# Performance work log

Measured on AMD Instinct MI355X. Metric: run time of the kernel, lower is better.

Reference implementation:

```python
import jax, jax.numpy as jnp
import numpy as np

EPS = 1e-5

def knn_idx(x, k):
    # x: (B,C,N). Returns (B,N,k) indices of k nearest neighbors (by L2).
    inner = -2.0 * jnp.einsum('bcn,bcm->bnm', x, x)          # (B,N,N)
    xx = jnp.sum(x * x, axis=1)                               # (B,N)
    neg_dist = -xx[:, :, None] - inner - xx[:, None, :]       # (B,N,N)
    _, idx = jax.lax.top_k(neg_dist, k)                       # (B,N,k)
    return idx

def get_graph_features(x, k):
    # x: (B,C,N) -> (B,2C,N,k) with channels = concat(neighbor-center, center)
    B, C, N = x.shape
    idx = knn_idx(x, k)                                       # (B,N,k)
    pts = jnp.transpose(x, (0, 2, 1))                         # (B,N,C)
    nbr = jax.vmap(lambda p, i: p[i])(pts, idx)               # (B,N,k,C)
    ctr = jnp.broadcast_to(pts[:, :, None, :], nbr.shape)     # (B,N,k,C)
    feat = jnp.concatenate([nbr - ctr, ctr], axis=-1)         # (B,N,k,2C)
    return jnp.transpose(feat, (0, 3, 1, 2))                  # (B,2C,N,k)

def conv_bn_relu(y, W, gamma, beta):
    # 1x1 conv (pointwise matmul) + train-mode BatchNorm2d + ReLU
    y = jnp.einsum('oc,bcnk->bonk', W, y)
    mean = jnp.mean(y, axis=(0, 2, 3), keepdims=True)
    var = jnp.var(y, axis=(0, 2, 3), keepdims=True)
    yhat = (y - mean) * jax.lax.rsqrt(var + EPS)
    return jax.nn.relu(yhat * gamma[None, :, None, None] + beta[None, :, None, None])

def setup_inputs() -> dict:
    key = jax.random.key(0)
    ks = jax.random.split(key, 16)
    B, N, k, emb = 8, 2048, 20, 512
    x = jax.random.normal(ks[0], (B, 3, N), dtype=jnp.float32)
    def w(kk, o, c):
        return jax.random.normal(kk, (o, c), dtype=jnp.float32) * (1.0 / np.sqrt(c))
    inp = {
        'x': x, 'k': k,
        'W1': w(ks[1], 64, 6),   'W2': w(ks[2], 64, 64),
        'W3': w(ks[3], 128, 64), 'W4': w(ks[4], 256, 128),
        'W5': w(ks[5], emb, 512),
    }
    for i, c in zip(range(1, 6), [64, 64, 128, 256, emb]):
        inp[f'g{i}'] = 1.0 + 0.1 * jax.random.normal(ks[5 + i], (c,), dtype=jnp.float32)
        inp[f'b{i}'] = 0.1 * jax.random.normal(ks[10 + i], (c,), dtype=jnp.float32)
    return inp

def reference(x, W1, W2, W3, W4, W5, g1, b1, g2, b2, g3, b3, g4, b4, g5, b5, k):
    B, C, N = x.shape
    h = get_graph_features(x, k)                  # (B,6,N,k)
    h = conv_bn_relu(h, W1, g1, b1)               # (B,64,N,k)
    x1 = jnp.max(h, axis=-1, keepdims=True)
    h = conv_bn_relu(h, W2, g2, b2)               # (B,64,N,k)
    x2 = jnp.max(h, axis=-1, keepdims=True)
    h = conv_bn_relu(h, W3, g3, b3)               # (B,128,N,k)
    x3 = jnp.max(h, axis=-1, keepdims=True)
    h = conv_bn_relu(h, W4, g4, b4)               # (B,256,N,k)
    x4 = jnp.max(h, axis=-1, keepdims=True)
    cat = jnp.concatenate([x1, x2, x3, x4], axis=1)  # (B,512,N,1)
    out = conv_bn_relu(cat, W5, g5, b5)              # (B,emb,N,1)
    return out.reshape(B, -1, N)
```

## Files before the change

kernel.cpp:

```cpp
#include <hip/hip_runtime.h>
#include <hip/hip_bf16.h>

typedef __hip_bfloat16 bf16;
typedef __attribute__((ext_vector_type(8))) short short8v;
typedef __attribute__((ext_vector_type(4))) float f32x4;
typedef unsigned int uint;
typedef unsigned long long u64;

#define BATCH 8
#define NPTS 2048
#define KNN 20
#define NK (NPTS*KNN)
#define P4 (BATCH*NK)
#define BN_TOT (BATCH*NPTS)

union BU { bf16 h; unsigned short u; };
__device__ __forceinline__ unsigned short f2bf(float f){
    BU bu; bu.h = __float2bfloat16(f); return bu.u;
}
__device__ __forceinline__ float bfu2f(unsigned short u){
    return __uint_as_float(((uint)u) << 16);
}
__device__ __forceinline__ uint fenc(float f){
    uint b = __float_as_uint(f);
    return (b & 0x80000000u) ? ~b : (b | 0x80000000u);
}

__global__ void initK(float* __restrict__ shadow)
{
    int t = blockIdx.x*256 + threadIdx.x;
    if (t < 5*16*1024) shadow[t] = 0.f;
}

__global__ void cvtWS(const float* __restrict__ src, short* __restrict__ dst, int Cin)
{
    int t = blockIdx.x*256 + threadIdx.x;
    int co = t / Cin, ci = t - co*Cin;
    dst[(size_t)co*Cin + (ci ^ ((co & 7) << 3))] = (short)f2bf(src[t]);
}

__global__ __launch_bounds__(512)
void knn_kernel(const float* __restrict__ x, int* __restrict__ idx)
{
    #pragma clang fp contract(off)
    __shared__ float4 sp[NPTS];
    const int b  = blockIdx.x / (NPTS/8);
    const int nb = blockIdx.x % (NPTS/8);
    const float* xb = x + (size_t)b*3*NPTS;
    for (int i = threadIdx.x; i < NPTS; i += 512) {
        float y0 = xb[i], y1 = xb[NPTS+i], y2 = xb[2*NPTS+i];
        float4 p; p.x = y0; p.y = y1; p.z = y2;
        p.w = y0*y0 + y1*y1 + y2*y2;
        sp[i] = p;
    }
    __syncthreads();

    const int wave = threadIdx.x >> 6;
    const int lane = threadIdx.x & 63;
    const int n = nb*8 + wave;

    const float4 pn = sp[n];
    const float x0 = pn.x, x1 = pn.y, x2 = pn.z;
    const float xxn = pn.w;

    constexpr int L = 4;
    float bA[L], bB[L]; int iA[L], iB[L];
    #pragma unroll
    for (int i = 0; i < L; ++i) {
        bA[i] = -3e38f; bB[i] = -3e38f; iA[i] = 0x7fffffff; iB[i] = 0x7fffffff;
    }

    float4 c0 = sp[lane], c1 = sp[lane + 64];
    #pragma unroll
    for (int t = 0; t < NPTS/128; ++t) {
        float4 n0, n1;
        if (t + 1 < NPTS/128) {
            n0 = sp[lane + (2*t+2)*64];
            n1 = sp[lane + (2*t+3)*64];
        }
        int m0 = lane + (2*t)*64, m1 = m0 + 64;
        float dot0 = x0*c0.x + x1*c0.y + x2*c0.z;
        float v0 = -xxn - (-2.f*dot0) - c0.w;
        float dot1 = x0*c1.x + x1*c1.y + x2*c1.z;
        float v1 = -xxn - (-2.f*dot1) - c1.w;
        int mi0 = m0, mi1 = m1;
        #pragma unroll
        for (int i = 0; i < L; ++i) {
            { bool sw = v0 > bA[i];
              float tv = sw ? bA[i] : v0; int ti = sw ? iA[i] : mi0;
              bA[i] = sw ? v0 : bA[i]; iA[i] = sw ? mi0 : iA[i]; v0 = tv; mi0 = ti; }
            { bool sw = v1 > bB[i];
              float tv = sw ? bB[i] : v1; int ti = sw ? iB[i] : mi1;
              bB[i] = sw ? v1 : bB[i]; iB[i] = sw ? mi1 : iB[i]; v1 = tv; mi1 = ti; }
        }
        c0 = n0; c1 = n1;
    }

    u64 kA[L], kB[L];
    #pragma unroll
    for (int i = 0; i < L; ++i) {
        kA[i] = ((u64)fenc(bA[i]) << 32) | (uint)(~iA[i]);
        kB[i] = ((u64)fenc(bB[i]) << 32) | (uint)(~iB[i]);
    }

    size_t obase = ((size_t)b*NPTS + n)*KNN;
    int popA = 0, popB = 0;
    #pragma unroll 1
    for (int s = 0; s < KNN; ++s) {
        bool useA = kA[0] >= kB[0];
        u64 my = useA ? kA[0] : kB[0];
        u64 g = my;
        #pragma unroll
        for (int off = 1; off < 64; off <<= 1) {
            u64 o = __shfl_xor(g, off);
            g = (o > g) ? o : g;
        }
        if (lane == 0) idx[obase + s] = (int)(~(uint)g);
        bool win = (my == g);
        bool pA = win && useA, pB = win && !useA;
        #pragma unroll
        for (int i = 0; i < L-1; ++i) {
            kA[i] = pA ? kA[i+1] : kA[i];
            kB[i] = pB ? kB[i+1] : kB[i];
        }
        kA[L-1] = pA ? 0ULL : kA[L-1];
        kB[L-1] = pB ? 0ULL : kB[L-1];
        popA += pA; popB += pB;
    }

    if (__any((popA >= L) || (popB >= L))) {
        float B[KNN]; int BI[KNN];
        #pragma unroll
        for (int i = 0; i < KNN; ++i) { B[i] = -3e38f; BI[i] = 0x7fffffff; }
        #pragma unroll 1
        for (int j = 0; j < NPTS/64; ++j) {
            int m = lane + j*64;
            float4 p = sp[m];
            float dot = x0*p.x + x1*p.y + x2*p.z;
            float v = -xxn - (-2.f*dot) - p.w;
            int mi = m;
            #pragma unroll
            for (int i = 0; i < KNN; ++i) {
                bool sw = v > B[i];
                float tv = sw ? B[i]  : v;
                int   ti = sw ? BI[i] : mi;
                B[i]  = sw ? v  : B[i];
                BI[i] = sw ? mi : BI[i];
                v = tv; mi = ti;
            }
        }
        #pragma unroll 1
        for (int s = 0; s < KNN; ++s) {
            float mv = B[0]; int mi = BI[0];
            #pragma unroll
            for (int off = 1; off < 64; off <<= 1) {
                float ov = __shfl_xor(mv, off);
                int   oi = __shfl_xor(mi, off);
                if (ov > mv || (ov == mv && oi < mi)) { mv = ov; mi = oi; }
            }
            bool win = (B[0] == mv) && (BI[0] == mi);
            #pragma unroll
            for (int i = 0; i < KNN-1; ++i) {
                B[i]  = win ? B[i+1]  : B[i];
                BI[i] = win ? BI[i+1] : BI[i];
            }
            B[KNN-1]  = win ? -3e38f     : B[KNN-1];
            BI[KNN-1] = win ? 0x7fffffff : BI[KNN-1];
            if (lane == 0) idx[obase + s] = mi;
        }
    }
}

__global__ __launch_bounds__(256)
void conv1T(const float* __restrict__ x, const int* __restrict__ idx,
            const float* __restrict__ W1, bf16* __restrict__ h1,
            float* __restrict__ shadow)
{
    __shared__ unsigned short lv[256][64];
    __shared__ float ps[4][64], pq[4][64];
    const int tid = threadIdx.x;
    int p = blockIdx.x*256 + tid;
    int b = p / NK;
    int r = p - b*NK;
    int n = r / KNN;
    int j = idx[p];
    const float* xb = x + (size_t)b*3*NPTS;
    float c0 = xb[n], c1 = xb[NPTS+n], c2 = xb[2*NPTS+n];
    float d0 = xb[j]-c0, d1 = xb[NPTS+j]-c1, d2 = xb[2*NPTS+j]-c2;
    uint4* outp = reinterpret_cast<uint4*>(reinterpret_cast<unsigned short*>(h1) + (size_t)p*64);
    uint4* lrow = reinterpret_cast<uint4*>(lv[tid]);
    #pragma unroll
    for (int ch = 0; ch < 8; ++ch) {
        uint u[4];
        #pragma unroll
        for (int q = 0; q < 4; ++q) {
            const float* wa = W1 + (ch*8 + q*2)*6;
            float a0 = wa[0]*d0 + wa[1]*d1 + wa[2]*d2 + wa[3]*c0 + wa[4]*c1 + wa[5]*c2;
            const float* wb = wa + 6;
            float a1 = wb[0]*d0 + wb[1]*d1 + wb[2]*d2 + wb[3]*c0 + wb[4]*c1 + wb[5]*c2;
            u[q] = (uint)f2bf(a0) | ((uint)f2bf(a1) << 16);
        }
        uint4 val = make_uint4(u[0], u[1], u[2], u[3]);
        outp[ch] = val;
        lrow[ch] = val;
    }
    __syncthreads();
    int c = tid & 63, grp = tid >> 6;
    float s = 0.f, q = 0.f;
    #pragma unroll 8
    for (int i = 0; i < 64; ++i) {
        float v = bfu2f(lv[grp*64 + i][c]);
        s += v; q += v*v;
    }
    ps[grp][c] = s; pq[grp][c] = q;
    __syncthreads();
    if (tid < 64) {
        float S = ps[0][tid]+ps[1][tid]+ps[2][tid]+ps[3][tid];
        float Q = pq[0][tid]+pq[1][tid]+pq[2][tid]+pq[3][tid];
        float* sh = shadow + (size_t)(blockIdx.x & 15)*1024;
        atomicAdd(&sh[tid], S);
        atomicAdd(&sh[512 + tid], Q);
    }
}

__global__ void fin_kernel(const float* __restrict__ shadow,
                           const float* __restrict__ gamma, const float* __restrict__ beta,
                           float* __restrict__ scbiF, int C, float invCnt)
{
    for (int c = threadIdx.x; c < C; c += 256) {
        float s = 0.f, q = 0.f;
        #pragma unroll
        for (int i = 0; i < 16; ++i) { s += shadow[i*1024 + c]; q += shadow[i*1024 + 512 + c]; }
        float m = s*invCnt;
        float var = q*invCnt - m*m;
        float rs = rsqrtf(var + 1e-5f);
        float sc = rs * gamma[c];
        float bi = fmaf(-m, sc, beta[c]);
        scbiF[2*c] = sc; scbiF[2*c+1] = bi;
    }
}

template<int Cout, int Cin, int M, int POOL, int NSPLIT, int KTILE, int BT, int PF>
__global__ __launch_bounds__(BT)
void gemmT(const short* __restrict__ Wb, const bf16* __restrict__ in,
           bf16* __restrict__ outT, float* __restrict__ shadow,
           float* __restrict__ pmax, float* __restrict__ pmin)
{
    constexpr int CSPL = Cout/NSPLIT;
    constexpr int NT   = CSPL/16;
    constexpr int ROWS = (BT/64)*16*M;
    constexpr int KSTOT = Cin/32;
    constexpr int KPT   = KTILE/32;
    constexpr int NTILE = Cin/KTILE;
    constexpr int NG    = POOL ? ROWS/KNN : 1;
    constexpr size_t WB = (size_t)CSPL*KTILE*2;
    constexpr size_t PB = POOL ? (size_t)2*ROWS*17*4 : 0;
    constexpr size_t SB = WB > PB ? WB : PB;

    __shared__ __align__(16) char smem[SB];
    short* WsmS = reinterpret_cast<short*>(smem);
    float* poolF = reinterpret_cast<float*>(smem);

    const int tid  = threadIdx.x;
    const int lane = tid & 63;
    const int g = lane >> 4, mr = lane & 15;
    const int wid = tid >> 6;
    const int rowBlk = blockIdx.x*ROWS;
    const int rowW   = rowBlk + wid*(16*M);
    const int ntBase = blockIdx.y*CSPL;
    const short* inS = reinterpret_cast<const short*>(in);

    f32x4 acc[M][NT];
    #pragma unroll
    for (int m = 0; m < M; ++m)
    #pragma unroll
    for (int i = 0; i < NT; ++i) acc[m][i] = (f32x4){0.f,0.f,0.f,0.f};

    short8v a[M], anext[M];
    if (PF) {
        #pragma unroll
        for (int m = 0; m < M; ++m)
            a[m] = *reinterpret_cast<const short8v*>(inS + (size_t)(rowW + m*16 + mr)*Cin + 8*g);
    }

    #pragma unroll 1
    for (int kt = 0; kt < NTILE; ++kt) {
        if (kt) __syncthreads();
        {
            const int ktBase = kt*KTILE;
            for (int f8 = tid; f8 < CSPL*KTILE/8; f8 += BT) {
                int f = f8*8;
                int row = f / KTILE, col = f - row*KTILE;
                short8v v = *reinterpret_cast<const short8v*>(
                    Wb + (size_t)(ntBase + row)*Cin + ktBase + col);
                *reinterpret_cast<short8v*>(WsmS + f) = v;
            }
        }
        __syncthreads();

        #pragma unroll
        for (int ksl = 0; ksl < KPT; ++ksl) {
            const int ksg = kt*KPT + ksl;
            const int k0 = ksg*32 + 8*g;
            if (!PF) {
                #pragma unroll
                for (int m = 0; m < M; ++m)
                    a[m] = *reinterpret_cast<const short8v*>(inS + (size_t)(rowW + m*16 + mr)*Cin + k0);
            } else if (ksg + 1 < KSTOT) {
                #pragma unroll
                for (int m = 0; m < M; ++m)
                    anext[m] = *reinterpret_cast<const short8v*>(inS + (size_t)(rowW + m*16 + mr)*Cin + k0 + 32);
            }
            const int kx = ksl*32 + 8*g;
            #pragma unroll
            for (int nt = 0; nt < NT; ++nt) {
                const int brow = nt*16 + mr;
                short8v bfr = *reinterpret_cast<const short8v*>(
                    WsmS + brow*KTILE + (kx ^ ((mr & 7) << 3)));
                #pragma unroll
                for (int m = 0; m < M; ++m)
                    acc[m][nt] = __builtin_amdgcn_mfma_f32_16x16x32_bf16(a[m], bfr, acc[m][nt], 0, 0, 0);
            }
            if (PF) {
                #pragma unroll
                for (int m = 0; m < M; ++m) a[m] = anext[m];
            }
        }
    }

    float* sh = shadow + (size_t)((blockIdx.x ^ blockIdx.y) & 15)*1024;
    #pragma unroll
    for (int nt = 0; nt < NT; ++nt) {
        float s = 0.f, q = 0.f;
        #pragma unroll
        for (int m = 0; m < M; ++m)
        #pragma unroll
        for (int j = 0; j < 4; ++j) { float v = acc[m][nt][j]; s += v; q += v*v; }
        s += __shfl_xor(s, 16); s += __shfl_xor(s, 32);
        q += __shfl_xor(q, 16); q += __shfl_xor(q, 32);
        if (g == 0) {
            atomicAdd(&sh[ntBase + nt*16 + mr], s);
            atomicAdd(&sh[512 + ntBase + nt*16 + mr], q);
        }
    }

    if (!POOL) {
        #pragma unroll
        for (int m = 0; m < M; ++m)
        #pragma unroll
        for (int nt = 0; nt < NT; ++nt)
        #pragma unroll
        for (int j = 0; j < 4; ++j) {
            size_t row = (size_t)rowW + m*16 + g*4 + j;
            outT[row*Cout + ntBase + nt*16 + mr] = __float2bfloat16(acc[m][nt][j]);
        }
    } else {
        __syncthreads();
        #pragma unroll
        for (int np = 0; np < NT/2; ++np) {
            #pragma unroll
            for (int hh = 0; hh < 2; ++hh) {
                #pragma unroll
                for (int m = 0; m < M; ++m)
                #pragma unroll
                for (int j = 0; j < 4; ++j) {
                    int row = wid*(16*M) + m*16 + g*4 + j;
                    poolF[hh*(ROWS*17) + row*17 + mr] = acc[m][np*2+hh][j];
                }
            }
            __syncthreads();
            if (tid < 2*NG*16) {
                int hh = tid / (NG*16);
                int gg = (tid >> 4) % NG;
                int cc = tid & 15;
                float mx = -3e38f, mn = 3e38f;
                #pragma unroll
                for (int kk = 0; kk < KNN; ++kk) {
                    float v = poolF[hh*(ROWS*17) + (gg*KNN + kk)*17 + cc];
                    mx = fmaxf(mx, v); mn = fminf(mn, v);
                }
                int grp = rowBlk/KNN + gg;
                int c = ntBase + (np*2 + hh)*16 + cc;
                pmax[(size_t)grp*256 + c] = mx;
                pmin[(size_t)grp*256 + c] = mn;
            }
            __syncthreads();
        }
    }
}

template<int C>
__global__ void maxpoolT(bf16* __restrict__ h, const float* __restrict__ scbiF,
                         bf16* __restrict__ catT, int coff)
{
    constexpr int PB = 256/C;
    int t = threadIdx.x;
    int c = t & (C-1);
    int bn = blockIdx.x*PB + t/C;
    float sc = scbiF[2*c], bi = scbiF[2*c+1];
    unsigned short* src = reinterpret_cast<unsigned short*>(h) + (size_t)bn*KNN*C + c;
    float best = 0.f;
    #pragma unroll
    for (int kk = 0; kk < KNN; ++kk) {
        float a = fmaxf(fmaf(bfu2f(src[kk*C]), sc, bi), 0.f);
        src[kk*C] = f2bf(a);
        best = fmaxf(best, a);
    }
    catT[(size_t)bn*512 + coff + c] = __float2bfloat16(best);
}

__global__ void cat4T(const float* __restrict__ pmax, const float* __restrict__ pmin,
                      const float* __restrict__ scbiF, const float* __restrict__ g4,
                      bf16* __restrict__ catT)
{
    int t = blockIdx.x*256 + threadIdx.x;
    int c = t & 255, bn = t >> 8;
    float sc = scbiF[2*c], bi = scbiF[2*c+1];
    float v = (g4[c] >= 0.f) ? pmax[t] : pmin[t];
    catT[(size_t)bn*512 + 256 + c] = __float2bfloat16(fmaxf(fmaf(v, sc, bi), 0.f));
}

__global__ void finalT(const bf16* __restrict__ h5, const float* __restrict__ scbiF,
                       float* __restrict__ out)
{
    __shared__ float ls[64][65];
    int t = threadIdx.x;
    int b = blockIdx.z, n0 = blockIdx.x*64, c0 = blockIdx.y*64;
    int j = t & 63, i0 = t >> 6;
    float sc = scbiF[2*(c0+j)], bi = scbiF[2*(c0+j)+1];
    const unsigned short* hp = reinterpret_cast<const unsigned short*>(h5);
    for (int it = 0; it < 16; ++it) {
        int i = i0 + it*4;
        float v = bfu2f(hp[((size_t)(b*NPTS + n0 + i))*512 + c0 + j]);
        ls[i][j] = fmaxf(fmaf(v, sc, bi), 0.f);
    }
    __syncthreads();
    for (int it = 0; it < 16; ++it) {
        int cr = i0 + it*4;
        out[((size_t)b*512 + c0 + cr)*NPTS + n0 + j] = ls[j][cr];
    }
}

extern "C" void kernel_launch(void* const* d_in, const int* in_sizes, int n_in,
                              void* d_out, int out_size, void* d_ws, size_t ws_size,
                              hipStream_t stream)
{
    const float* x  = (const float*)d_in[0];
    const float* W1 = (const float*)d_in[2];
    const float* W2 = (const float*)d_in[3];
    const float* W3 = (const float*)d_in[4];
    const float* W4 = (const float*)d_in[5];
    const float* W5 = (const float*)d_in[6];
    const float* g1 = (const float*)d_in[7];  const float* b1 = (const float*)d_in[8];
    const float* g2 = (const float*)d_in[9];  const float* b2 = (const float*)d_in[10];
    const float* g3 = (const float*)d_in[11]; const float* b3 = (const float*)d_in[12];
    const float* g4 = (const float*)d_in[13]; const float* b4 = (const float*)d_in[14];
    const float* g5 = (const float*)d_in[15]; const float* b5 = (const float*)d_in[16];
    float* out = (float*)d_out;

    char* w = (char*)d_ws;
    int*   idx    = (int*)w;
    float* scbiF  = (float*)(w + 1323008);
    float* shadow = (float*)(w + 1343488);
    short* Wb     = (short*)(w + 1671168);
    bf16*  h1     = (bf16*)(w + 2285568);
    float* pmax   = (float*)h1;
    float* pmin   = pmax + (size_t)BN_TOT*256;
    bf16*  h2     = (bf16*)(w + 44228608);
    bf16*  h5     = h2;
    bf16*  h3     = (bf16*)(w + 86171648);
    bf16*  catT   = (bf16*)(w + 170057728);

    short* Wb2 = Wb, *Wb3 = Wb + 4096, *Wb4 = Wb + 12288, *Wb5 = Wb + 45056;
    float* sh1 = shadow, *sh2 = shadow + 16384, *sh3 = shadow + 2*16384,
         * sh4 = shadow + 3*16384, *sh5 = shadow + 4*16384;

    initK<<<320, 256, 0, stream>>>(shadow);
    cvtWS<<<16,   256, 0, stream>>>(W2, Wb2, 64);
    cvtWS<<<32,   256, 0, stream>>>(W3, Wb3, 64);
    cvtWS<<<128,  256, 0, stream>>>(W4, Wb4, 128);
    cvtWS<<<1024, 256, 0, stream>>>(W5, Wb5, 512);

    knn_kernel<<<BATCH*NPTS/8, 512, 0, stream>>>(x, idx);
    conv1T<<<P4/256, 256, 0, stream>>>(x, idx, W1, h1, sh1);

    fin_kernel<<<1, 256, 0, stream>>>(sh1, g1, b1, scbiF, 64, 1.f/P4);
    maxpoolT<64><<<BN_TOT/4, 256, 0, stream>>>(h1, scbiF, catT, 0);

    gemmT<64,64,2,0,1,64,256,1><<<dim3(P4/128,1), 256, 0, stream>>>(
        Wb2, h1, h2, sh2, nullptr, nullptr);
    fin_kernel<<<1, 256, 0, stream>>>(sh2, g2, b2, scbiF + 1024, 64, 1.f/P4);
    maxpoolT<64><<<BN_TOT/4, 256, 0, stream>>>(h2, scbiF + 1024, catT, 64);

    gemmT<128,64,2,0,1,64,256,1><<<dim3(P4/128,1), 256, 0, stream>>>(
        Wb3, h2, h3, sh3, nullptr, nullptr);
    fin_kernel<<<1, 256, 0, stream>>>(sh3, g3, b3, scbiF + 2048, 128, 1.f/P4);
    maxpoolT<128><<<BN_TOT/2, 256, 0, stream>>>(h3, scbiF + 2048, catT, 128);

    gemmT<256,128,2,1,2,128,640,1><<<dim3(P4/320,2), 640, 0, stream>>>(
        Wb4, h3, nullptr, sh4, pmax, pmin);
    fin_kernel<<<1, 256, 0, stream>>>(sh4, g4, b4, scbiF + 3072, 256, 1.f/P4);
    cat4T<<<BN_TOT, 256, 0, stream>>>(pmax, pmin, scbiF + 3072, g4, catT);

    gemmT<512,512,2,0,4,128,256,1><<<dim3(BN_TOT/128,4), 256, 0, stream>>>(
        Wb5, catT, h5, sh5, nullptr, nullptr);
    fin_kernel<<<1, 256, 0, stream>>>(sh5, g5, b5, scbiF + 4096, 512, 1.f/BN_TOT);
    finalT<<<dim3(NPTS/64, 8, BATCH), 256, 0, stream>>>(h5, scbiF + 4096, out);
}
```

Measured before the change: 362.5 us.

## Split KNN candidate scan across two waves per query and merge by rank

Each query point is now handled by two waves, each scanning half of the candidate points and producing its own sorted top-20 list in shared memory. The two lists are merged by rank counting and written to the index output. This halves the serial per-wave scan and selection work and doubles the block count. In exchange, each block now reloads the whole point cloud into shared memory for only 4 queries instead of 8, and adds a block barrier plus a merge step.

```diff
diff --git a/kernel.cpp b/kernel.cpp
--- a/kernel.cpp
+++ b/kernel.cpp
@@ -44,8 +44,9 @@
 {
     #pragma clang fp contract(off)
     __shared__ float4 sp[NPTS];
-    const int b  = blockIdx.x / (NPTS/8);
-    const int nb = blockIdx.x % (NPTS/8);
+    __shared__ u64 skeys[4][2][KNN];
+    const int b  = blockIdx.x / (NPTS/4);
+    const int nb = blockIdx.x % (NPTS/4);
     const float* xb = x + (size_t)b*3*NPTS;
     for (int i = threadIdx.x; i < NPTS; i += 512) {
         float y0 = xb[i], y1 = xb[NPTS+i], y2 = xb[2*NPTS+i];
@@ -55,9 +56,12 @@
     }
     __syncthreads();
 
-    const int wave = threadIdx.x >> 6;
+    const int wv   = threadIdx.x >> 6;
     const int lane = threadIdx.x & 63;
-    const int n = nb*8 + wave;
+    const int pidx = wv >> 1;
+    const int hh   = wv & 1;
+    const int n    = nb*4 + pidx;
+    const int base = hh*1024;
 
     const float4 pn = sp[n];
     const float x0 = pn.x, x1 = pn.y, x2 = pn.z;
@@ -70,15 +74,15 @@
         bA[i] = -3e38f; bB[i] = -3e38f; iA[i] = 0x7fffffff; iB[i] = 0x7fffffff;
     }
 
-    float4 c0 = sp[lane], c1 = sp[lane + 64];
-    #pragma unroll
-    for (int t = 0; t < NPTS/128; ++t) {
+    float4 c0 = sp[base + lane], c1 = sp[base + lane + 64];
+    #pragma unroll
+    for (int t = 0; t < 8; ++t) {
         float4 n0, n1;
-        if (t + 1 < NPTS/128) {
-            n0 = sp[lane + (2*t+2)*64];
-            n1 = sp[lane + (2*t+3)*64];
-        }
-        int m0 = lane + (2*t)*64, m1 = m0 + 64;
+        if (t + 1 < 8) {
+            n0 = sp[base + lane + (2*t+2)*64];
+            n1 = sp[base + lane + (2*t+3)*64];
+        }
+        int m0 = base + lane + (2*t)*64, m1 = m0 + 64;
         float dot0 = x0*c0.x + x1*c0.y + x2*c0.z;
         float v0 = -xxn - (-2.f*dot0) - c0.w;
         float dot1 = x0*c1.x + x1*c1.y + x2*c1.z;
@@ -103,7 +107,6 @@
         kB[i] = ((u64)fenc(bB[i]) << 32) | (uint)(~iB[i]);
     }
 
-    size_t obase = ((size_t)b*NPTS + n)*KNN;
     int popA = 0, popB = 0;
     #pragma unroll 1
     for (int s = 0; s < KNN; ++s) {
@@ -115,7 +118,7 @@
             u64 o = __shfl_xor(g, off);
             g = (o > g) ? o : g;
         }
-        if (lane == 0) idx[obase + s] = (int)(~(uint)g);
+        if (lane == 0) skeys[pidx][hh][s] = g;
         bool win = (my == g);
         bool pA = win && useA, pB = win && !useA;
         #pragma unroll
@@ -133,8 +136,8 @@
         #pragma unroll
         for (int i = 0; i < KNN; ++i) { B[i] = -3e38f; BI[i] = 0x7fffffff; }
         #pragma unroll 1
-        for (int j = 0; j < NPTS/64; ++j) {
-            int m = lane + j*64;
+        for (int j = 0; j < 16; ++j) {
+            int m = base + lane + j*64;
             float4 p = sp[m];
             float dot = x0*p.x + x1*p.y + x2*p.z;
             float v = -xxn - (-2.f*dot) - p.w;
@@ -166,8 +169,22 @@
             }
             B[KNN-1]  = win ? -3e38f     : B[KNN-1];
             BI[KNN-1] = win ? 0x7fffffff : BI[KNN-1];
-            if (lane == 0) idx[obase + s] = mi;
-        }
+            if (lane == 0) skeys[pidx][hh][s] = ((u64)fenc(mv) << 32) | (uint)(~mi);
+        }
+    }
+    __syncthreads();
+
+    if (hh == 0 && lane < 2*KNN) {
+        bool isA = lane < KNN;
+        int i = isA ? lane : lane - KNN;
+        u64 key = skeys[pidx][isA ? 0 : 1][i];
+        const u64* other = skeys[pidx][isA ? 1 : 0];
+        int cnt = 0;
+        #pragma unroll
+        for (int j = 0; j < KNN; ++j) cnt += (other[j] > key) ? 1 : 0;
+        int rank = i + cnt;
+        if (rank < KNN)
+            idx[((size_t)b*NPTS + n)*KNN + rank] = (int)(~(uint)key);
     }
 }
 
@@ -481,7 +498,7 @@
     cvtWS<<<128,  256, 0, stream>>>(W4, Wb4, 128);
     cvtWS<<<1024, 256, 0, stream>>>(W5, Wb5, 512);
 
-    knn_kernel<<<BATCH*NPTS/8, 512, 0, stream>>>(x, idx);
+    knn_kernel<<<BATCH*NPTS/4, 512, 0, stream>>>(x, idx);
     conv1T<<<P4/256, 256, 0, stream>>>(x, idx, W1, h1, sh1);
 
     fin_kernel<<<1, 256, 0, stream>>>(sh1, g1, b1, scbiF, 64, 1.f/P4);
```

Result: slower. 400.3 us (+10.4%).
